# Optimization experiments

Measured on AMD Instinct MI355X. Metric: run time of the kernel, lower is better.

Reference implementation:

```python
import jax, jax.numpy as jnp
import numpy as np

D = 64
H = 4
HD = D // H
N_MOL, E_MOL = 2048, 32768
N_PROT, E_PROT = 8192, 262144
LN_EPS = 1e-5


def _lin_params(key, d_in, d_out):
    k1, k2 = jax.random.split(key)
    lim = 1.0 / np.sqrt(d_in)
    w = jax.random.uniform(k1, (d_in, d_out), minval=-lim, maxval=lim, dtype=jnp.float32)
    b = jax.random.uniform(k2, (d_out,), minval=-lim, maxval=lim, dtype=jnp.float32)
    return w, b


def setup_inputs() -> dict:
    key = jax.random.key(0)
    ks = jax.random.split(key, 20)
    inp = {
        'x_mol': jax.random.normal(ks[0], (N_MOL, D), dtype=jnp.float32),
        'edge_index_mol': jax.random.randint(ks[1], (2, E_MOL), 0, N_MOL),
        'edge_attr_mol': jax.random.normal(ks[2], (E_MOL, D), dtype=jnp.float32),
        'x_prot': jax.random.normal(ks[3], (N_PROT, D), dtype=jnp.float32),
        'edge_index_prot': jax.random.randint(ks[4], (2, E_PROT), 0, N_PROT),
        'edge_attr_prot': jax.random.normal(ks[5], (E_PROT, D), dtype=jnp.float32),
    }
    # GINE MLPs: Linear -> ReLU -> Linear
    inp['mol_w1'], inp['mol_b1'] = _lin_params(ks[6], D, D)
    inp['mol_w2'], inp['mol_b2'] = _lin_params(ks[7], D, D)
    inp['prot_w1'], inp['prot_b1'] = _lin_params(ks[8], D, D)
    inp['prot_w2'], inp['prot_b2'] = _lin_params(ks[9], D, D)
    # cross-attn mol->prot (query=mol, key/value=prot)
    inp['mp_wq'], inp['mp_bq'] = _lin_params(ks[10], D, D)
    inp['mp_wk'], inp['mp_bk'] = _lin_params(ks[11], D, D)
    inp['mp_wv'], inp['mp_bv'] = _lin_params(ks[12], D, D)
    # cross-attn prot->mol (query=prot, key/value=mol)
    inp['pm_wq'], inp['pm_bq'] = _lin_params(ks[13], D, D)
    inp['pm_wk'], inp['pm_bk'] = _lin_params(ks[14], D, D)
    inp['pm_wv'], inp['pm_bv'] = _lin_params(ks[15], D, D)
    # layer norms
    inp['ln_mol_g'] = jnp.ones((D,), jnp.float32)
    inp['ln_mol_b'] = jnp.zeros((D,), jnp.float32)
    inp['ln_prot_g'] = jnp.ones((D,), jnp.float32)
    inp['ln_prot_b'] = jnp.zeros((D,), jnp.float32)
    return inp


def _gine_conv(x, edge_index, edge_attr, w1, b1, w2, b2, n_nodes):
    # message: relu(x_j + edge_attr); aggregate: mean at target; update: MLP((1+eps)*x + aggr), eps=0
    src, dst = edge_index[0], edge_index[1]
    msg = jax.nn.relu(x[src] + edge_attr)                       # [E, D]
    ssum = jax.ops.segment_sum(msg, dst, num_segments=n_nodes)  # [N, D]
    cnt = jax.ops.segment_sum(jnp.ones((msg.shape[0],), msg.dtype), dst, num_segments=n_nodes)
    aggr = ssum / jnp.maximum(cnt, 1.0)[:, None]
    h = x + aggr
    h = jax.nn.relu(h @ w1 + b1) @ w2 + b2
    return h


def _cross_attn(q_nodes, k_nodes, wq, bq, wk, bk, wv, bv):
    Nq, Nk = q_nodes.shape[0], k_nodes.shape[0]
    Q = (q_nodes @ wq + bq).reshape(Nq, H, HD)
    K = (k_nodes @ wk + bk).reshape(Nk, H, HD)
    V = (k_nodes @ wv + bv).reshape(Nk, H, HD)
    scores = jnp.einsum('qhd,khd->hqk', Q, K) / np.sqrt(HD).astype(np.float32)
    attn = jax.nn.softmax(scores, axis=-1)                      # [H, Nq, Nk]
    out = jnp.einsum('hqk,khd->qhd', attn, V).reshape(Nq, D)
    return out


def _layer_norm(x, g, b):
    mu = jnp.mean(x, axis=-1, keepdims=True)
    var = jnp.mean(jnp.square(x - mu), axis=-1, keepdims=True)
    return (x - mu) * jax.lax.rsqrt(var + LN_EPS) * g + b


def reference(x_mol, edge_index_mol, edge_attr_mol, x_prot, edge_index_prot, edge_attr_prot,
              mol_w1, mol_b1, mol_w2, mol_b2, prot_w1, prot_b1, prot_w2, prot_b2,
              mp_wq, mp_bq, mp_wk, mp_bk, mp_wv, mp_bv,
              pm_wq, pm_bq, pm_wk, pm_bk, pm_wv, pm_bv,
              ln_mol_g, ln_mol_b, ln_prot_g, ln_prot_b):
    h_mol = jax.nn.relu(_gine_conv(x_mol, edge_index_mol, edge_attr_mol,
                                   mol_w1, mol_b1, mol_w2, mol_b2, x_mol.shape[0]))
    h_prot = jax.nn.relu(_gine_conv(x_prot, edge_index_prot, edge_attr_prot,
                                    prot_w1, prot_b1, prot_w2, prot_b2, x_prot.shape[0]))
    h_mol_attn = _cross_attn(h_mol, h_prot, mp_wq, mp_bq, mp_wk, mp_bk, mp_wv, mp_bv)
    h_prot_attn = _cross_attn(h_prot, h_mol, pm_wq, pm_bq, pm_wk, pm_bk, pm_wv, pm_bv)
    out_mol = _layer_norm(h_mol + h_mol_attn, ln_mol_g, ln_mol_b)
    out_prot = _layer_norm(h_prot + h_prot_attn, ln_prot_g, ln_prot_b)
    return out_mol, out_prot
```

## Files before the change

### kernel.cpp

```cpp
#include <hip/hip_runtime.h>

#define NM 2048
#define EM 32768
#define NP 8192
#define EP 262144

typedef __attribute__((ext_vector_type(8))) short short8;
typedef __attribute__((ext_vector_type(4))) float f32x4;

#define LOG2E 1.44269504088896340736f

__device__ __forceinline__ float e2(float x) { return __builtin_amdgcn_exp2f(x); }
__device__ __forceinline__ unsigned int pk_bf16(float a, float b) {
    unsigned int ua = __float_as_uint(a) + 0x8000u;
    unsigned int ub = __float_as_uint(b) + 0x8000u;
    return __builtin_amdgcn_perm(ua, ub, 0x03020706u);
}
__device__ __forceinline__ unsigned short cvt_bf16(float f) {
    unsigned int u = __float_as_uint(f);
    u = (u + 0x7fff + ((u >> 16) & 1)) >> 16;
    return (unsigned short)u;
}

__global__ __launch_bounds__(256) void hist_kernel(
    const int* __restrict__ ei_m, const int* __restrict__ ei_p,
    int* __restrict__ cnt_m, int* __restrict__ cnt_p)
{
    int idx = blockIdx.x * 256 + threadIdx.x;
    if (idx < EM) atomicAdd(&cnt_m[ei_m[EM + idx]], 1);
    int j = idx - EM;
    if (j >= 0 && j < EP) atomicAdd(&cnt_p[ei_p[EP + j]], 1);
}

__global__ __launch_bounds__(256) void scan_kernel(
    const int* __restrict__ cnt_m, const int* __restrict__ cnt_p,
    int* __restrict__ start_m, int* __restrict__ start_p,
    int* __restrict__ cur_m, int* __restrict__ cur_p)
{
    const int* cnt; int* start; int* cur; int n;
    if (blockIdx.x == 0) { cnt = cnt_m; start = start_m; cur = cur_m; n = NM; }
    else                 { cnt = cnt_p; start = start_p; cur = cur_p; n = NP; }
    int per = n >> 8;
    int tid = threadIdx.x;
    int base = tid * per;
    int s = 0;
    for (int i = 0; i < per; i++) s += cnt[base + i];
    __shared__ int wsum[4];
    int lane = tid & 63, w = tid >> 6;
    int v = s;
    #pragma unroll
    for (int off = 1; off < 64; off <<= 1) {
        int u = __shfl_up(v, off, 64);
        if (lane >= off) v += u;
    }
    if (lane == 63) wsum[w] = v;
    __syncthreads();
    int wo = 0;
    for (int i = 0; i < w; i++) wo += wsum[i];
    int run = wo + v - s;
    for (int i = 0; i < per; i++) {
        start[base + i] = run; cur[base + i] = run;
        run += cnt[base + i];
    }
    if (tid == 255) start[n] = run;
}

__global__ __launch_bounds__(256) void scatter_kernel(
    const int* __restrict__ ei_m, const int* __restrict__ ei_p,
    int* __restrict__ cur_m, int* __restrict__ cur_p,
    int* __restrict__ pidx_m, int* __restrict__ pidx_p)
{
    int idx = blockIdx.x * 256 + threadIdx.x;
    if (idx < EM) {
        int d = ei_m[EM + idx];
        int pos = atomicAdd(&cur_m[d], 1);
        pidx_m[pos] = (idx << 11) | ei_m[idx];
    }
    int j = idx - EM;
    if (j >= 0 && j < EP) {
        int d = ei_p[EP + j];
        int pos = atomicAdd(&cur_p[d], 1);
        pidx_p[pos] = (j << 13) | ei_p[j];
    }
}

__global__ __launch_bounds__(256) void node_aggr_kernel(
    const float* __restrict__ x_m, const float* __restrict__ ea_m,
    const int* __restrict__ start_m, const int* __restrict__ pidx_m,
    const float* __restrict__ x_p, const float* __restrict__ ea_p,
    const int* __restrict__ start_p, const int* __restrict__ pidx_p,
    float* __restrict__ h0_m, float* __restrict__ h0_p)
{
    int wave = threadIdx.x >> 6, lane = threadIdx.x & 63;
    int slot = lane >> 4, dq = lane & 15;
    int nid = blockIdx.x * 4 + wave;
    const float *x, *ea; const int *start, *pidx; float* h0; int n, sh, msk;
    if (nid < NM) { x = x_m; ea = ea_m; start = start_m; pidx = pidx_m; h0 = h0_m; n = nid; sh = 11; msk = 2047; }
    else          { x = x_p; ea = ea_p; start = start_p; pidx = pidx_p; h0 = h0_p; n = nid - NM; sh = 13; msk = 8191; }
    int b = start[n], e = start[n + 1];
    int deg = e - b;
    const int* pp = pidx + b;
    float4 acc = {0.f, 0.f, 0.f, 0.f};
    for (int j = 0; j < deg; j += 4) {
        int jj = j + slot;
        if (jj < deg) {
            int v = pp[jj];
            const float4 a = *(const float4*)(ea + (size_t)(((unsigned)v) >> sh) * 64 + dq * 4);
            const float4 y = *(const float4*)(x + (size_t)(v & msk) * 64 + dq * 4);
            acc.x += fmaxf(y.x + a.x, 0.f);
            acc.y += fmaxf(y.y + a.y, 0.f);
            acc.z += fmaxf(y.z + a.z, 0.f);
            acc.w += fmaxf(y.w + a.w, 0.f);
        }
    }
    #pragma unroll
    for (int off = 16; off <= 32; off <<= 1) {
        acc.x += __shfl_xor(acc.x, off, 64);
        acc.y += __shfl_xor(acc.y, off, 64);
        acc.z += __shfl_xor(acc.z, off, 64);
        acc.w += __shfl_xor(acc.w, off, 64);
    }
    if (slot == 0) {
        float dinv = 1.0f / fmaxf((float)deg, 1.0f);
        const float4 xv = *(const float4*)(x + (size_t)n * 64 + dq * 4);
        float4 o;
        o.x = xv.x + acc.x * dinv;
        o.y = xv.y + acc.y * dinv;
        o.z = xv.z + acc.z * dinv;
        o.w = xv.w + acc.w * dinv;
        *(float4*)(h0 + (size_t)n * 64 + dq * 4) = o;
    }
}

__global__ __launch_bounds__(256) void gine_mlp_kernel(
    const float* __restrict__ h0_m, const float* __restrict__ h0_p,
    const float* __restrict__ w1m, const float* __restrict__ b1m,
    const float* __restrict__ w2m, const float* __restrict__ b2m,
    const float* __restrict__ w1p, const float* __restrict__ b1p,
    const float* __restrict__ w2p, const float* __restrict__ b2p,
    float* __restrict__ hm, float* __restrict__ hp)
{
    const float *h0, *w1, *b1, *w2, *b2; float* out; int row0;
    if (blockIdx.x < NM / 16) {
        h0 = h0_m; w1 = w1m; b1 = b1m; w2 = w2m; b2 = b2m; out = hm;
        row0 = blockIdx.x * 16;
    } else {
        h0 = h0_p; w1 = w1p; b1 = b1p; w2 = w2p; b2 = b2p; out = hp;
        row0 = (blockIdx.x - NM / 16) * 16;
    }
    __shared__ float sW1[4096], sW2[4096], sb1[64], sb2[64];
    __shared__ float sh0[16][64], sh1[16][64];
    int t = threadIdx.x;
    for (int i = t; i < 4096; i += 256) { sW1[i] = w1[i]; sW2[i] = w2[i]; }
    if (t < 64) { sb1[t] = b1[t]; sb2[t] = b2[t]; }
    for (int i = t; i < 16 * 64; i += 256) {
        int r = i >> 6, c = i & 63;
        sh0[r][c] = h0[(size_t)(row0 + r) * 64 + c];
    }
    __syncthreads();
    int j = t & 63, rs = t >> 6;
    for (int r = rs; r < 16; r += 4) {
        float a = sb1[j];
        #pragma unroll
        for (int c = 0; c < 64; c++) a += sh0[r][c] * sW1[c * 64 + j];
        sh1[r][j] = fmaxf(a, 0.0f);
    }
    __syncthreads();
    for (int r = rs; r < 16; r += 4) {
        float a = sb2[j];
        #pragma unroll
        for (int c = 0; c < 64; c++) a += sh1[r][c] * sW2[c * 64 + j];
        out[(size_t)(row0 + r) * 64 + j] = fmaxf(a, 0.0f);
    }
}

__global__ __launch_bounds__(256) void qkv_bf16_kernel(
    const float* __restrict__ hm, const float* __restrict__ hp,
    const float* __restrict__ wq_m, const float* __restrict__ bq_m,
    const float* __restrict__ wk_m, const float* __restrict__ bk_m,
    const float* __restrict__ wv_m, const float* __restrict__ bv_m,
    const float* __restrict__ wq_p, const float* __restrict__ bq_p,
    const float* __restrict__ wk_p, const float* __restrict__ bk_p,
    const float* __restrict__ wv_p, const float* __restrict__ bv_p,
    unsigned short* __restrict__ Qm, unsigned short* __restrict__ Km, unsigned short* __restrict__ Vtm,
    unsigned short* __restrict__ Qp, unsigned short* __restrict__ Kp, unsigned short* __restrict__ Vtp,
    int* __restrict__ norms)
{
    const float *x, *wq, *bq, *wk, *bk, *wv, *bv;
    unsigned short *Q, *K, *Vt; int row0, N, nbase;
    if (blockIdx.x < NM / 16) {
        x = hm; wq = wq_m; bq = bq_m; wk = wk_m; bk = bk_m; wv = wv_m; bv = bv_m;
        Q = Qm; K = Km; Vt = Vtm; N = NM; row0 = blockIdx.x * 16; nbase = 0;
    } else {
        x = hp; wq = wq_p; bq = bq_p; wk = wk_p; bk = bk_p; wv = wv_p; bv = bv_p;
        Q = Qp; K = Kp; Vt = Vtp; N = NP; row0 = (blockIdx.x - NM / 16) * 16; nbase = 2;
    }
    __shared__ float sWq[4096], sWk[4096], sWv[4096];
    __shared__ float sbq[64], sbk[64], sbv[64];
    __shared__ float sh0[16][64];
    __shared__ float rmx[8];
    int t = threadIdx.x;
    for (int i = t; i < 4096; i += 256) { sWq[i] = wq[i]; sWk[i] = wk[i]; sWv[i] = wv[i]; }
    if (t < 64) { sbq[t] = bq[t]; sbk[t] = bk[t]; sbv[t] = bv[t]; }
    for (int i = t; i < 16 * 64; i += 256) {
        int r = i >> 6, c = i & 63;
        sh0[r][c] = x[(size_t)(row0 + r) * 64 + c];
    }
    __syncthreads();
    int j = t & 63, rs = t >> 6;
    float qmx = 0.f, kmx = 0.f;
    for (int r = rs; r < 16; r += 4) {
        float aq = sbq[j], ak = sbk[j], av = sbv[j];
        #pragma unroll
        for (int c = 0; c < 64; c++) {
            float h = sh0[r][c];
            aq += h * sWq[c * 64 + j];
            ak += h * sWk[c * 64 + j];
            av += h * sWv[c * 64 + j];
        }
        float qs = aq * (0.25f * LOG2E);
        size_t o = (size_t)(row0 + r) * 64 + j;
        Q[o] = cvt_bf16(qs);
        K[o] = cvt_bf16(ak);
        Vt[(size_t)j * N + row0 + r] = cvt_bf16(av);
        float qsq = qs * qs, ksq = ak * ak;
        #pragma unroll
        for (int o2 = 1; o2 <= 8; o2 <<= 1) {
            qsq += __shfl_xor(qsq, o2, 64);
            ksq += __shfl_xor(ksq, o2, 64);
        }
        qmx = fmaxf(qmx, qsq);
        kmx = fmaxf(kmx, ksq);
    }
    qmx = fmaxf(qmx, __shfl_xor(qmx, 16, 64)); qmx = fmaxf(qmx, __shfl_xor(qmx, 32, 64));
    kmx = fmaxf(kmx, __shfl_xor(kmx, 16, 64)); kmx = fmaxf(kmx, __shfl_xor(kmx, 32, 64));
    if (j == 0) { rmx[rs] = qmx; rmx[4 + rs] = kmx; }
    __syncthreads();
    if (t == 0) {
        float q4 = fmaxf(fmaxf(rmx[0], rmx[1]), fmaxf(rmx[2], rmx[3]));
        float k4 = fmaxf(fmaxf(rmx[4], rmx[5]), fmaxf(rmx[6], rmx[7]));
        atomicMax(&norms[nbase],     __float_as_int(sqrtf(q4)));
        atomicMax(&norms[nbase + 1], __float_as_int(sqrtf(k4)));
    }
}

__global__ __launch_bounds__(256) void attn_kernel(
    const unsigned short* __restrict__ Qm, const unsigned short* __restrict__ Km,
    const unsigned short* __restrict__ Vtm,
    const unsigned short* __restrict__ Qp, const unsigned short* __restrict__ Kp,
    const unsigned short* __restrict__ Vtp,
    const int* __restrict__ norms, float* __restrict__ partial)
{
    __shared__ unsigned int plds[4][2][16][20];
    int t = threadIdx.x;
    int wave = t >> 6;
    int lane = t & 63;
    int qrow = lane & 15;
    int quad = lane >> 4;
    int T = blockIdx.x * 4 + wave;

    const unsigned short *Q, *K, *Vt; int Nk, ncb, tloc; float m;
    if (T < 4096) { Q = Qm; K = Kp; Vt = Vtp; Nk = NP; ncb = 3; tloc = T;
                    m = __int_as_float(norms[0]) * __int_as_float(norms[3]); }
    else          { Q = Qp; K = Km; Vt = Vtm; Nk = NM; ncb = 1; tloc = T - 4096;
                    m = __int_as_float(norms[2]) * __int_as_float(norms[1]); }
    int chunk = tloc & ((1 << ncb) - 1);
    int tmp = tloc >> ncb;
    int h = tmp & 3;
    int qt = tmp >> 2;

    short8 qf = {};
    if (quad < 2)
        qf = *(const short8*)(Q + ((size_t)(qt * 16 + qrow)) * 64 + h * 16 + quad * 8);

    const f32x4 zero4 = {0.f, 0.f, 0.f, 0.f};
    int kbase = chunk * 1024;
    const unsigned short* krow = K + (size_t)(kbase + qrow) * 64 + h * 16 + quad * 8;
    const unsigned short* vrow = Vt + ((size_t)(h * 16 + qrow)) * Nk + kbase + quad * 8;

    float l = 0.0f;
    f32x4 acc = zero4;

    short8 kf0p[2], kf1p[2], vfp[2];
    #pragma unroll
    for (int i = 0; i < 2; ++i) {
        kf0p[i] = (short8){}; kf1p[i] = (short8){};
        if (quad < 2) {
            kf0p[i] = *(const short8*)(krow + (size_t)(i * 32) * 64);
            kf1p[i] = *(const short8*)(krow + (size_t)(i * 32 + 16) * 64);
        }
        vfp[i] = *(const short8*)(vrow + i * 32);
    }

    #pragma unroll 2
    for (int it = 0; it < 32; ++it) {
        short8 kf0 = kf0p[it & 1], kf1 = kf1p[it & 1], vf = vfp[it & 1];
        if (it < 30) {
            int off = (it + 2) * 32;
            if (quad < 2) {
                kf0p[it & 1] = *(const short8*)(krow + (size_t)off * 64);
                kf1p[it & 1] = *(const short8*)(krow + (size_t)(off + 16) * 64);
            }
            vfp[it & 1] = *(const short8*)(vrow + off);
        }

        f32x4 s0 = __builtin_amdgcn_mfma_f32_16x16x32_bf16(kf0, qf, zero4, 0, 0, 0);
        f32x4 s1 = __builtin_amdgcn_mfma_f32_16x16x32_bf16(kf1, qf, zero4, 0, 0, 0);

        float p00 = e2(s0.x - m), p01 = e2(s0.y - m);
        float p02 = e2(s0.z - m), p03 = e2(s0.w - m);
        float p10 = e2(s1.x - m), p11 = e2(s1.y - m);
        float p12 = e2(s1.z - m), p13 = e2(s1.w - m);
        l += (((p00 + p01) + (p02 + p03)) + ((p10 + p11) + (p12 + p13)));

        uint2 w0; w0.x = pk_bf16(p00, p01); w0.y = pk_bf16(p02, p03);
        uint2 w1; w1.x = pk_bf16(p10, p11); w1.y = pk_bf16(p12, p13);
        *(uint2*)&plds[wave][it & 1][qrow][quad * 2] = w0;
        *(uint2*)&plds[wave][it & 1][qrow][8 + quad * 2] = w1;
        short8 pf = *(short8*)&plds[wave][it & 1][qrow][quad * 4];

        acc = __builtin_amdgcn_mfma_f32_16x16x32_bf16(vf, pf, acc, 0, 0, 0);
    }

    float ltot = l + __shfl_xor(l, 16, 64);
    ltot += __shfl_xor(ltot, 32, 64);

    float* pb = partial + (size_t)T * 288;
    *(f32x4*)&pb[qrow * 16 + quad * 4] = acc;
    if (quad == 0) { pb[256 + qrow] = m; pb[272 + qrow] = ltot; }
}

__global__ __launch_bounds__(256) void merge_ln_kernel(
    const float* __restrict__ partial,
    const float* __restrict__ h_m, const float* __restrict__ h_p,
    const float* __restrict__ gm, const float* __restrict__ bm,
    const float* __restrict__ gp, const float* __restrict__ bp_,
    float* __restrict__ out)
{
    int t = threadIdx.x;
    int grow = blockIdx.x * 4 + (t >> 6);
    int c = t & 63;
    const float *pbase, *hbuf, *g, *bb; float* o; int NC, row;
    if (grow < NM) { pbase = partial;               hbuf = h_m; g = gm; bb = bm;  o = out;             NC = 8; row = grow; }
    else           { pbase = partial + 4096 * 288;  hbuf = h_p; g = gp; bb = bp_; o = out + NM * 64;   NC = 2; row = grow - NM; }
    int hi = c >> 4, d = c & 15;
    int qt = row >> 4, ql = row & 15;
    const float* base = pbase + (size_t)(qt * 4 + hi) * NC * 288;
    float M = -3.0e38f;
    for (int cc = 0; cc < NC; ++cc) M = fmaxf(M, base[cc * 288 + 256 + ql]);
    float L = 0.0f, A = 0.0f;
    for (int cc = 0; cc < NC; ++cc) {
        float w = e2(base[cc * 288 + 256 + ql] - M);
        L += base[cc * 288 + 272 + ql] * w;
        A += base[cc * 288 + ql * 16 + d] * w;
    }
    float v = hbuf[(size_t)row * 64 + c] + A / L;
    float s = v;
    #pragma unroll
    for (int o2 = 32; o2 >= 1; o2 >>= 1) s += __shfl_xor(s, o2, 64);
    float mu = s * (1.0f / 64.0f);
    float dv = v - mu;
    float sq = dv * dv;
    #pragma unroll
    for (int o2 = 32; o2 >= 1; o2 >>= 1) sq += __shfl_xor(sq, o2, 64);
    float var = sq * (1.0f / 64.0f);
    o[(size_t)row * 64 + c] = dv * rsqrtf(var + 1e-5f) * g[c] + bb[c];
}

extern "C" void kernel_launch(void* const* d_in, const int* in_sizes, int n_in,
                              void* d_out, int out_size, void* d_ws, size_t ws_size,
                              hipStream_t stream)
{
    const float* x_mol   = (const float*)d_in[0];
    const int*   ei_mol  = (const int*)  d_in[1];
    const float* ea_mol  = (const float*)d_in[2];
    const float* x_prot  = (const float*)d_in[3];
    const int*   ei_prot = (const int*)  d_in[4];
    const float* ea_prot = (const float*)d_in[5];
    const float* mol_w1  = (const float*)d_in[6];
    const float* mol_b1  = (const float*)d_in[7];
    const float* mol_w2  = (const float*)d_in[8];
    const float* mol_b2  = (const float*)d_in[9];
    const float* prot_w1 = (const float*)d_in[10];
    const float* prot_b1 = (const float*)d_in[11];
    const float* prot_w2 = (const float*)d_in[12];
    const float* prot_b2 = (const float*)d_in[13];
    const float* mp_wq = (const float*)d_in[14]; const float* mp_bq = (const float*)d_in[15];
    const float* mp_wk = (const float*)d_in[16]; const float* mp_bk = (const float*)d_in[17];
    const float* mp_wv = (const float*)d_in[18]; const float* mp_bv = (const float*)d_in[19];
    const float* pm_wq = (const float*)d_in[20]; const float* pm_bq = (const float*)d_in[21];
    const float* pm_wk = (const float*)d_in[22]; const float* pm_bk = (const float*)d_in[23];
    const float* pm_wv = (const float*)d_in[24]; const float* pm_bv = (const float*)d_in[25];
    const float* ln_mol_g  = (const float*)d_in[26];
    const float* ln_mol_b  = (const float*)d_in[27];
    const float* ln_prot_g = (const float*)d_in[28];
    const float* ln_prot_b = (const float*)d_in[29];

    float* ws = (float*)d_ws;
    float* h_mol   = ws;
    float* h_prot  = h_mol + 131072;
    float* partial = h_prot + 524288;
    float* h0_mol  = partial;
    float* h0_prot = h0_mol + 131072;
    int* ip      = (int*)(partial + 2359296);
    int* cnt_m   = ip;
    int* cnt_p   = cnt_m + 2048;
    int* norms   = cnt_p + 8192;
    int* start_m = norms + 4;
    int* start_p = start_m + 2052;
    int* cur_m   = start_p + 8196;
    int* cur_p   = cur_m + 2048;
    int* pidx_m  = cur_p + 8192;
    int* pidx_p  = pidx_m + 32768;
    unsigned short* bf = (unsigned short*)(pidx_p + 262144);
    unsigned short* Qm  = bf;
    unsigned short* Km  = Qm + 131072;
    unsigned short* Vtm = Km + 131072;
    unsigned short* Qp  = Vtm + 131072;
    unsigned short* Kp  = Qp + 524288;
    unsigned short* Vtp = Kp + 524288;

    hipMemsetAsync(cnt_m, 0, (size_t)(2048 + 8192 + 4) * sizeof(int), stream);

    const int EB = (EM + EP) / 256;
    hist_kernel<<<EB, 256, 0, stream>>>(ei_mol, ei_prot, cnt_m, cnt_p);
    scan_kernel<<<2, 256, 0, stream>>>(cnt_m, cnt_p, start_m, start_p, cur_m, cur_p);
    scatter_kernel<<<EB, 256, 0, stream>>>(ei_mol, ei_prot, cur_m, cur_p, pidx_m, pidx_p);
    node_aggr_kernel<<<(NM + NP) / 4, 256, 0, stream>>>(
        x_mol, ea_mol, start_m, pidx_m,
        x_prot, ea_prot, start_p, pidx_p, h0_mol, h0_prot);

    gine_mlp_kernel<<<(NM + NP) / 16, 256, 0, stream>>>(
        h0_mol, h0_prot, mol_w1, mol_b1, mol_w2, mol_b2,
        prot_w1, prot_b1, prot_w2, prot_b2, h_mol, h_prot);

    qkv_bf16_kernel<<<(NM + NP) / 16, 256, 0, stream>>>(
        h_mol, h_prot,
        mp_wq, mp_bq, pm_wk, pm_bk, pm_wv, pm_bv,
        pm_wq, pm_bq, mp_wk, mp_bk, mp_wv, mp_bv,
        Qm, Km, Vtm, Qp, Kp, Vtp, norms);

    attn_kernel<<<2048, 256, 0, stream>>>(Qm, Km, Vtm, Qp, Kp, Vtp, norms, partial);

    float* out = (float*)d_out;
    merge_ln_kernel<<<(NM + NP) / 4, 256, 0, stream>>>(
        partial, h_mol, h_prot, ln_mol_g, ln_mol_b, ln_prot_g, ln_prot_b, out);
}
```

Measured before the change: 336.7 us.

## Use wave-uniform edge gathers and keep the attention P tile in registers

The node aggregation kernel now gives each wave one node, reads the edge indices as scalars through readfirstlane, and has each lane own one feature column, unrolling the edge loop by eight for memory-level parallelism. The attention kernel drops the LDS round-trip for the probability tile: V is loaded as two 4-element halves so the MFMA k-ordering matches the in-register P layout, and bf16 packing becomes truncation instead of rounding. K fragments are now loaded by all quads instead of only two, so the zero-padded K positions are no longer zero, though they still multiply zero-padded Q. Truncating P to bf16 adds a small bias in precision.

```diff
diff --git a/kernel.cpp b/kernel.cpp
--- a/kernel.cpp
+++ b/kernel.cpp
@@ -6,15 +6,14 @@
 #define EP 262144
 
 typedef __attribute__((ext_vector_type(8))) short short8;
+typedef __attribute__((ext_vector_type(4))) short short4v;
 typedef __attribute__((ext_vector_type(4))) float f32x4;
 
 #define LOG2E 1.44269504088896340736f
 
 __device__ __forceinline__ float e2(float x) { return __builtin_amdgcn_exp2f(x); }
-__device__ __forceinline__ unsigned int pk_bf16(float a, float b) {
-    unsigned int ua = __float_as_uint(a) + 0x8000u;
-    unsigned int ub = __float_as_uint(b) + 0x8000u;
-    return __builtin_amdgcn_perm(ua, ub, 0x03020706u);
+__device__ __forceinline__ unsigned int pk_bf16_tr(float a, float b) {
+    return __builtin_amdgcn_perm(__float_as_uint(a), __float_as_uint(b), 0x03020706u);
 }
 __device__ __forceinline__ unsigned short cvt_bf16(float f) {
     unsigned int u = __float_as_uint(f);
@@ -92,44 +91,52 @@
     float* __restrict__ h0_m, float* __restrict__ h0_p)
 {
     int wave = threadIdx.x >> 6, lane = threadIdx.x & 63;
-    int slot = lane >> 4, dq = lane & 15;
     int nid = blockIdx.x * 4 + wave;
     const float *x, *ea; const int *start, *pidx; float* h0; int n, sh, msk;
     if (nid < NM) { x = x_m; ea = ea_m; start = start_m; pidx = pidx_m; h0 = h0_m; n = nid; sh = 11; msk = 2047; }
     else          { x = x_p; ea = ea_p; start = start_p; pidx = pidx_p; h0 = h0_p; n = nid - NM; sh = 13; msk = 8191; }
-    int b = start[n], e = start[n + 1];
+    int b  = __builtin_amdgcn_readfirstlane(start[n]);
+    int e  = __builtin_amdgcn_readfirstlane(start[n + 1]);
     int deg = e - b;
     const int* pp = pidx + b;
-    float4 acc = {0.f, 0.f, 0.f, 0.f};
-    for (int j = 0; j < deg; j += 4) {
-        int jj = j + slot;
-        if (jj < deg) {
-            int v = pp[jj];
-            const float4 a = *(const float4*)(ea + (size_t)(((unsigned)v) >> sh) * 64 + dq * 4);
-            const float4 y = *(const float4*)(x + (size_t)(v & msk) * 64 + dq * 4);
-            acc.x += fmaxf(y.x + a.x, 0.f);
-            acc.y += fmaxf(y.y + a.y, 0.f);
-            acc.z += fmaxf(y.z + a.z, 0.f);
-            acc.w += fmaxf(y.w + a.w, 0.f);
-        }
-    }
-    #pragma unroll
-    for (int off = 16; off <= 32; off <<= 1) {
-        acc.x += __shfl_xor(acc.x, off, 64);
-        acc.y += __shfl_xor(acc.y, off, 64);
-        acc.z += __shfl_xor(acc.z, off, 64);
-        acc.w += __shfl_xor(acc.w, off, 64);
-    }
-    if (slot == 0) {
-        float dinv = 1.0f / fmaxf((float)deg, 1.0f);
-        const float4 xv = *(const float4*)(x + (size_t)n * 64 + dq * 4);
-        float4 o;
-        o.x = xv.x + acc.x * dinv;
-        o.y = xv.y + acc.y * dinv;
-        o.z = xv.z + acc.z * dinv;
-        o.w = xv.w + acc.w * dinv;
-        *(float4*)(h0 + (size_t)n * 64 + dq * 4) = o;
-    }
+    float acc = 0.f;
+    int j = 0;
+    for (; j + 8 <= deg; j += 8) {
+        int v0 = __builtin_amdgcn_readfirstlane(pp[j]);
+        int v1 = __builtin_amdgcn_readfirstlane(pp[j + 1]);
+        int v2 = __builtin_amdgcn_readfirstlane(pp[j + 2]);
+        int v3 = __builtin_amdgcn_readfirstlane(pp[j + 3]);
+        int v4 = __builtin_amdgcn_readfirstlane(pp[j + 4]);
+        int v5 = __builtin_amdgcn_readfirstlane(pp[j + 5]);
+        int v6 = __builtin_amdgcn_readfirstlane(pp[j + 6]);
+        int v7 = __builtin_amdgcn_readfirstlane(pp[j + 7]);
+        float a0 = ea[(size_t)(((unsigned)v0) >> sh) * 64 + lane];
+        float a1 = ea[(size_t)(((unsigned)v1) >> sh) * 64 + lane];
+        float a2 = ea[(size_t)(((unsigned)v2) >> sh) * 64 + lane];
+        float a3 = ea[(size_t)(((unsigned)v3) >> sh) * 64 + lane];
+        float a4 = ea[(size_t)(((unsigned)v4) >> sh) * 64 + lane];
+        float a5 = ea[(size_t)(((unsigned)v5) >> sh) * 64 + lane];
+        float a6 = ea[(size_t)(((unsigned)v6) >> sh) * 64 + lane];
+        float a7 = ea[(size_t)(((unsigned)v7) >> sh) * 64 + lane];
+        float y0 = x[(size_t)(v0 & msk) * 64 + lane];
+        float y1 = x[(size_t)(v1 & msk) * 64 + lane];
+        float y2 = x[(size_t)(v2 & msk) * 64 + lane];
+        float y3 = x[(size_t)(v3 & msk) * 64 + lane];
+        float y4 = x[(size_t)(v4 & msk) * 64 + lane];
+        float y5 = x[(size_t)(v5 & msk) * 64 + lane];
+        float y6 = x[(size_t)(v6 & msk) * 64 + lane];
+        float y7 = x[(size_t)(v7 & msk) * 64 + lane];
+        acc += fmaxf(y0 + a0, 0.f); acc += fmaxf(y1 + a1, 0.f);
+        acc += fmaxf(y2 + a2, 0.f); acc += fmaxf(y3 + a3, 0.f);
+        acc += fmaxf(y4 + a4, 0.f); acc += fmaxf(y5 + a5, 0.f);
+        acc += fmaxf(y6 + a6, 0.f); acc += fmaxf(y7 + a7, 0.f);
+    }
+    for (; j < deg; ++j) {
+        int v0 = __builtin_amdgcn_readfirstlane(pp[j]);
+        acc += fmaxf(x[(size_t)(v0 & msk) * 64 + lane] + ea[(size_t)(((unsigned)v0) >> sh) * 64 + lane], 0.f);
+    }
+    float aggr = acc / fmaxf((float)deg, 1.f);
+    h0[(size_t)n * 64 + lane] = x[(size_t)n * 64 + lane] + aggr;
 }
 
 __global__ __launch_bounds__(256) void gine_mlp_kernel(
@@ -251,13 +258,11 @@
     const unsigned short* __restrict__ Vtp,
     const int* __restrict__ norms, float* __restrict__ partial)
 {
-    __shared__ unsigned int plds[4][2][16][20];
     int t = threadIdx.x;
-    int wave = t >> 6;
     int lane = t & 63;
     int qrow = lane & 15;
     int quad = lane >> 4;
-    int T = blockIdx.x * 4 + wave;
+    int T = blockIdx.x * 4 + (t >> 6);
 
     const unsigned short *Q, *K, *Vt; int Nk, ncb, tloc; float m;
     if (T < 4096) { Q = Qm; K = Kp; Vt = Vtp; Nk = NP; ncb = 3; tloc = T;
@@ -276,32 +281,31 @@
     const f32x4 zero4 = {0.f, 0.f, 0.f, 0.f};
     int kbase = chunk * 1024;
     const unsigned short* krow = K + (size_t)(kbase + qrow) * 64 + h * 16 + quad * 8;
-    const unsigned short* vrow = Vt + ((size_t)(h * 16 + qrow)) * Nk + kbase + quad * 8;
-
-    float l = 0.0f;
+    const unsigned short* vrow = Vt + ((size_t)(h * 16 + qrow)) * Nk + kbase + quad * 4;
+
+    float la = 0.0f, lb = 0.0f;
     f32x4 acc = zero4;
 
-    short8 kf0p[2], kf1p[2], vfp[2];
+    short8 kf0p[2], kf1p[2];
+    short4v vap[2], vbp[2];
     #pragma unroll
     for (int i = 0; i < 2; ++i) {
-        kf0p[i] = (short8){}; kf1p[i] = (short8){};
-        if (quad < 2) {
-            kf0p[i] = *(const short8*)(krow + (size_t)(i * 32) * 64);
-            kf1p[i] = *(const short8*)(krow + (size_t)(i * 32 + 16) * 64);
-        }
-        vfp[i] = *(const short8*)(vrow + i * 32);
+        kf0p[i] = *(const short8*)(krow + (size_t)(i * 32) * 64);
+        kf1p[i] = *(const short8*)(krow + (size_t)(i * 32 + 16) * 64);
+        vap[i] = *(const short4v*)(vrow + i * 32);
+        vbp[i] = *(const short4v*)(vrow + i * 32 + 16);
     }
 
     #pragma unroll 2
     for (int it = 0; it < 32; ++it) {
-        short8 kf0 = kf0p[it & 1], kf1 = kf1p[it & 1], vf = vfp[it & 1];
+        short8 kf0 = kf0p[it & 1], kf1 = kf1p[it & 1];
+        short4v va = vap[it & 1], vb = vbp[it & 1];
         if (it < 30) {
             int off = (it + 2) * 32;
-            if (quad < 2) {
-                kf0p[it & 1] = *(const short8*)(krow + (size_t)off * 64);
-                kf1p[it & 1] = *(const short8*)(krow + (size_t)(off + 16) * 64);
-            }
-            vfp[it & 1] = *(const short8*)(vrow + off);
+            kf0p[it & 1] = *(const short8*)(krow + (size_t)off * 64);
+            kf1p[it & 1] = *(const short8*)(krow + (size_t)(off + 16) * 64);
+            vap[it & 1] = *(const short4v*)(vrow + off);
+            vbp[it & 1] = *(const short4v*)(vrow + off + 16);
         }
 
         f32x4 s0 = __builtin_amdgcn_mfma_f32_16x16x32_bf16(kf0, qf, zero4, 0, 0, 0);
@@ -311,17 +315,22 @@
         float p02 = e2(s0.z - m), p03 = e2(s0.w - m);
         float p10 = e2(s1.x - m), p11 = e2(s1.y - m);
         float p12 = e2(s1.z - m), p13 = e2(s1.w - m);
-        l += (((p00 + p01) + (p02 + p03)) + ((p10 + p11) + (p12 + p13)));
-
-        uint2 w0; w0.x = pk_bf16(p00, p01); w0.y = pk_bf16(p02, p03);
-        uint2 w1; w1.x = pk_bf16(p10, p11); w1.y = pk_bf16(p12, p13);
-        *(uint2*)&plds[wave][it & 1][qrow][quad * 2] = w0;
-        *(uint2*)&plds[wave][it & 1][qrow][8 + quad * 2] = w1;
-        short8 pf = *(short8*)&plds[wave][it & 1][qrow][quad * 4];
+        la += (p00 + p01) + (p02 + p03);
+        lb += (p10 + p11) + (p12 + p13);
+
+        short8 pf;
+        ((unsigned int*)&pf)[0] = pk_bf16_tr(p00, p01);
+        ((unsigned int*)&pf)[1] = pk_bf16_tr(p02, p03);
+        ((unsigned int*)&pf)[2] = pk_bf16_tr(p10, p11);
+        ((unsigned int*)&pf)[3] = pk_bf16_tr(p12, p13);
+        short8 vf;
+        *(short4v*)&vf = va;
+        *((short4v*)&vf + 1) = vb;
 
         acc = __builtin_amdgcn_mfma_f32_16x16x32_bf16(vf, pf, acc, 0, 0, 0);
     }
 
+    float l = la + lb;
     float ltot = l + __shfl_xor(l, 16, 64);
     ltot += __shfl_xor(ltot, 32, 64);
 
```

New measurement: 381.1 us. 13.2% more time.
